# Kernel tuning notes

Hardware: AMD Instinct MI355X
Metric: run time of the kernel (lower is better)

## Reference

```python
import jax, jax.numpy as jnp
import numpy as np
from jax import lax


def _normalizer(x):
    # faithful to: x / norm(x, axis=-1, keepdims=True) + 1e-10
    return x / jnp.linalg.norm(x, axis=-1, keepdims=True) + 1e-10


def setup_inputs() -> dict:
    key = jax.random.key(0)
    k1, k2, k3, k4 = jax.random.split(key, 4)
    Q, D, N, C = 4096, 768, 100000, 1000
    return {
        "feature": jax.random.normal(k1, (Q, D), dtype=jnp.float32),
        "logit": jax.random.normal(k2, (Q, C), dtype=jnp.float32),
        "bank_feas": jax.random.normal(k3, (N, D), dtype=jnp.float32),
        "bank_logits": jax.random.normal(k4, (N, C), dtype=jnp.float32),
        "K": 100,
    }


def reference(feature, logit, bank_feas, bank_logits, K):
    # --- setup(): build bank_guide ---
    bank_confs = jax.nn.logsumexp(bank_logits, axis=-1)          # [N]
    bank_guide = _normalizer(bank_feas) * bank_confs[:, None]    # [N, D]

    # --- forward() ---
    feas_norm = _normalizer(feature)                             # [Q, D]
    energy = jax.nn.logsumexp(logit, axis=-1)                    # [Q]

    # exact kNN inner-product search (faiss IndexFlatIP) = GEMM + top-k
    sims = jnp.einsum("qd,nd->qn", feas_norm, bank_guide)        # [Q, N]
    topk_vals, _ = lax.top_k(sims, K)                            # [Q, K]
    conf = jnp.mean(topk_vals, axis=-1)                          # [Q]

    score = conf * energy
    return -score
```

## Files before the change

### kernel.cpp

```cpp
#include <hip/hip_runtime.h>
#include <hip/hip_bf16.h>

#define QROWS 4096
#define DDIM  768
#define NBANK 100000
#define CDIM  1000
#define KTOP  100
#define NPAD  102400
#define SEGW2 12800
#define LCAP2 4096

typedef float floatx4 __attribute__((ext_vector_type(4)));
typedef short bf16x8 __attribute__((ext_vector_type(8)));

__device__ inline ushort f2bf(float f) {
  uint b = __float_as_uint(f);
  uint r = b + 0x7fffu + ((b >> 16) & 1u);
  return (ushort)(r >> 16);
}
__device__ inline float o16f(ushort u) {
  ushort b = (u & 0x8000) ? (ushort)(u & 0x7fff) : (ushort)~u;
  return __uint_as_float((uint)b << 16);
}

__global__ __launch_bounds__(256) void bank_prep(const float* __restrict__ logits,
                                                 const float* __restrict__ feas,
                                                 ushort* __restrict__ b16) {
  int row = blockIdx.x * 4 + (threadIdx.x >> 6);
  int lane = threadIdx.x & 63;
  if (row >= NPAD) return;
  ushort4* dst = (ushort4*)(b16 + (size_t)row * DDIM);
  if (row >= NBANK) {
#pragma unroll
    for (int j = 0; j < 3; j++) dst[lane + j * 64] = make_ushort4(0, 0, 0, 0);
    return;
  }
  const float4* lp = (const float4*)(logits + (size_t)row * CDIM);
  float4 v[4];
  float m = -3.0e38f;
#pragma unroll
  for (int j = 0; j < 4; j++) {
    int idx = lane + j * 64;
    if (idx < CDIM / 4) {
      v[j] = lp[idx];
      m = fmaxf(m, fmaxf(fmaxf(v[j].x, v[j].y), fmaxf(v[j].z, v[j].w)));
    } else {
      v[j] = make_float4(-3.0e38f, -3.0e38f, -3.0e38f, -3.0e38f);
    }
  }
#pragma unroll
  for (int off = 32; off; off >>= 1) m = fmaxf(m, __shfl_xor(m, off));
  float s = 0.f;
#pragma unroll
  for (int j = 0; j < 4; j++)
    s += __expf(v[j].x - m) + __expf(v[j].y - m) +
         __expf(v[j].z - m) + __expf(v[j].w - m);
#pragma unroll
  for (int off = 32; off; off >>= 1) s += __shfl_xor(s, off);
  float conf = m + __logf(s);
  const float4* fp = (const float4*)(feas + (size_t)row * DDIM);
  float4 w[3];
  float ss = 0.f;
#pragma unroll
  for (int j = 0; j < 3; j++) {
    w[j] = fp[lane + j * 64];
    ss += w[j].x * w[j].x + w[j].y * w[j].y + w[j].z * w[j].z + w[j].w * w[j].w;
  }
#pragma unroll
  for (int off = 32; off; off >>= 1) ss += __shfl_xor(ss, off);
  float scale = conf / sqrtf(ss);
#pragma unroll
  for (int j = 0; j < 3; j++)
    dst[lane + j * 64] = make_ushort4(f2bf(w[j].x * scale), f2bf(w[j].y * scale),
                                      f2bf(w[j].z * scale), f2bf(w[j].w * scale));
}

__global__ __launch_bounds__(256) void lse_rows(const float* __restrict__ x,
                                                float* __restrict__ out,
                                                int nrows, int ncols) {
  int row = blockIdx.x * 4 + (threadIdx.x >> 6);
  int lane = threadIdx.x & 63;
  if (row >= nrows) return;
  const float4* rp = (const float4*)(x + (size_t)row * ncols);
  int n4 = ncols >> 2;
  float4 v[4];
  float m = -3.0e38f;
#pragma unroll
  for (int j = 0; j < 4; j++) {
    int idx = lane + j * 64;
    if (idx < n4) {
      v[j] = rp[idx];
      m = fmaxf(m, fmaxf(fmaxf(v[j].x, v[j].y), fmaxf(v[j].z, v[j].w)));
    } else {
      v[j] = make_float4(-3.0e38f, -3.0e38f, -3.0e38f, -3.0e38f);
    }
  }
#pragma unroll
  for (int off = 32; off; off >>= 1) m = fmaxf(m, __shfl_xor(m, off));
  float s = 0.f;
#pragma unroll
  for (int j = 0; j < 4; j++)
    s += __expf(v[j].x - m) + __expf(v[j].y - m) +
         __expf(v[j].z - m) + __expf(v[j].w - m);
#pragma unroll
  for (int off = 32; off; off >>= 1) s += __shfl_xor(s, off);
  if (lane == 0) out[row] = m + __logf(s);
}

__global__ __launch_bounds__(256) void feat_norm(const float* __restrict__ x,
                                                 ushort* __restrict__ y) {
  int row = blockIdx.x * 4 + (threadIdx.x >> 6);
  int lane = threadIdx.x & 63;
  if (row >= QROWS) return;
  const float4* rp = (const float4*)(x + (size_t)row * DDIM);
  float4 v[3];
  float ss = 0.f;
#pragma unroll
  for (int j = 0; j < 3; j++) {
    v[j] = rp[lane + j * 64];
    ss += v[j].x * v[j].x + v[j].y * v[j].y + v[j].z * v[j].z + v[j].w * v[j].w;
  }
#pragma unroll
  for (int off = 32; off; off >>= 1) ss += __shfl_xor(ss, off);
  float rn = 1.0f / sqrtf(ss);
  ushort4* dst = (ushort4*)(y + (size_t)row * DDIM);
#pragma unroll
  for (int j = 0; j < 3; j++)
    dst[lane + j * 64] = make_ushort4(f2bf(v[j].x * rn), f2bf(v[j].y * rn),
                                      f2bf(v[j].z * rn), f2bf(v[j].w * rn));
}

#define GBM 256
#define GBN 256
#define GBK 64
#define NT  (DDIM / GBK)
#define GNWG ((QROWS / GBM) * (NPAD / GBN))

__device__ inline void load_lds16(const void* g, void* l) {
  __builtin_amdgcn_global_load_lds(
      (const __attribute__((address_space(1))) void*)g,
      (__attribute__((address_space(3))) void*)l, 16, 0, 0);
}

__global__ __launch_bounds__(512, 2) void gemm_sims(const ushort* __restrict__ A,
                                                    const ushort* __restrict__ B,
                                                    ushort* __restrict__ C) {
  __shared__ ushort lds[2 * 32768];
  const int tid = threadIdx.x;
  const int lane = tid & 63;
  const int wid = tid >> 6;
  const int wm = wid >> 2, wn = wid & 3;
  const int lr = lane & 15, lg = lane >> 4;

  int flat = blockIdx.x;
  int wgid = (flat & 7) * (GNWG / 8) + (flat >> 3);
  int sup = wgid >> 4, wi = wgid & 15;
  int q_idx = (sup & 3) * 4 + (wi & 3);
  int n_idx = (sup >> 2) * 4 + (wi >> 2);
  const int qBase = q_idx * GBM;
  const int nBase = n_idx * GBN;

  const int rin = lane >> 3;
  const int cswu = ((lane & 7) ^ rin) << 3;

  auto stageA = [&](int t, int buf) {
#pragma unroll
    for (int r = 0; r < 4; r++) {
      int G = r * 8 + wid;
      int row = qBase + G * 8 + rin;
      load_lds16(A + (size_t)row * DDIM + t * GBK + cswu,
                 lds + buf * 32768 + G * 512 + lane * 8);
    }
  };
  auto stageB = [&](int t, int buf) {
#pragma unroll
    for (int r = 0; r < 4; r++) {
      int G = r * 8 + wid;
      int row = nBase + G * 8 + rin;
      load_lds16(B + (size_t)row * DDIM + t * GBK + cswu,
                 lds + buf * 32768 + 16384 + G * 512 + lane * 8);
    }
  };

  floatx4 acc[8][4] = {};
  const int rsw = (lr & 7) << 3;

  stageA(0, 0); stageB(0, 0); stageA(1, 1); stageB(1, 1);

  for (int s = 0; s < NT; s++) {
    const int buf = s & 1;
    if (s == 0)           asm volatile("s_waitcnt vmcnt(8)" ::: "memory");
    else if (s == NT - 1) asm volatile("s_waitcnt vmcnt(0)" ::: "memory");
    else                  asm volatile("s_waitcnt vmcnt(4)" ::: "memory");
    __builtin_amdgcn_s_barrier();
    __builtin_amdgcn_sched_barrier(0);
    if (s >= 1 && s + 1 < NT) stageA(s + 1, buf ^ 1);
    const ushort* Ab = lds + buf * 32768;
    const ushort* Bb = Ab + 16384;

    bf16x8 bfr[4][2], af[2][2];
#pragma unroll
    for (int n = 0; n < 4; n++)
#pragma unroll
      for (int kk = 0; kk < 2; kk++)
        bfr[n][kk] = *(const bf16x8*)(Bb + (wn * 64 + n * 16 + lr) * 64 +
                                      ((kk * 32 + lg * 8) ^ rsw));
#pragma unroll
    for (int m = 0; m < 2; m++)
#pragma unroll
      for (int kk = 0; kk < 2; kk++)
        af[m][kk] = *(const bf16x8*)(Ab + (wm * 128 + m * 16 + lr) * 64 +
                                     ((kk * 32 + lg * 8) ^ rsw));
    __builtin_amdgcn_s_setprio(1);
#pragma unroll
    for (int m = 0; m < 2; m++)
#pragma unroll
      for (int n = 0; n < 4; n++)
#pragma unroll
        for (int kk = 0; kk < 2; kk++)
          acc[m][n] = __builtin_amdgcn_mfma_f32_16x16x32_bf16(af[m][kk], bfr[n][kk],
                                                              acc[m][n], 0, 0, 0);
    __builtin_amdgcn_s_setprio(0);
    __builtin_amdgcn_s_barrier();
    __builtin_amdgcn_sched_barrier(0);
    if (s + 2 < NT) stageB(s + 2, buf);

#pragma unroll
    for (int q = 1; q < 4; q++) {
      bf16x8 aq[2][2];
#pragma unroll
      for (int m = 0; m < 2; m++)
#pragma unroll
        for (int kk = 0; kk < 2; kk++)
          aq[m][kk] = *(const bf16x8*)(Ab + (wm * 128 + (2 * q + m) * 16 + lr) * 64 +
                                       ((kk * 32 + lg * 8) ^ rsw));
      __builtin_amdgcn_s_setprio(1);
#pragma unroll
      for (int m = 0; m < 2; m++)
#pragma unroll
        for (int n = 0; n < 4; n++)
#pragma unroll
          for (int kk = 0; kk < 2; kk++)
            acc[2 * q + m][n] = __builtin_amdgcn_mfma_f32_16x16x32_bf16(
                aq[m][kk], bfr[n][kk], acc[2 * q + m][n], 0, 0, 0);
      __builtin_amdgcn_s_setprio(0);
    }
  }

#pragma unroll
  for (int m = 0; m < 8; m++)
#pragma unroll
    for (int n = 0; n < 4; n++) {
      int q = qBase + wm * 128 + m * 16 + lg * 4;
      int col = nBase + wn * 64 + n * 16 + lr;
      ushort* cp = C + (size_t)q * NPAD + col;
#pragma unroll
      for (int r = 0; r < 4; r++) cp[(size_t)r * NPAD] = f2bf(acc[m][n][r]);
    }
}

__global__ __launch_bounds__(256) void topk_seg(const ushort* __restrict__ sims,
                                                ushort* __restrict__ cand) {
  __shared__ ushort smax[256];
  __shared__ ushort list[LCAP2];
  __shared__ int shC, shM, ipart[4];
  const int t = threadIdx.x;
  const int lane = t & 63;
  const int q = blockIdx.x >> 3, seg = blockIdx.x & 7;
  const ushort* base = sims + (size_t)q * NPAD + seg * SEGW2;

  uint v[25];
#pragma unroll
  for (int i = 0; i < 6; i++) {
    uint4 w = ((const uint4*)base)[i * 256 + t];
    uint ww[4] = {w.x, w.y, w.z, w.w};
#pragma unroll
    for (int e = 0; e < 4; e++) {
      uint u = ww[e];
      uint mm = ((u >> 15) & 0x00010001u) * 0xffffu;
      v[4 * i + e] = (u ^ mm) | (0x80008000u & ~mm);
    }
    if (seg == 7 && (i * 256 + t) >= 1300) {
      v[4 * i] = 0; v[4 * i + 1] = 0; v[4 * i + 2] = 0; v[4 * i + 3] = 0;
    }
  }
  {
    if (seg == 7) {
      v[24] = 0;
    } else {
      uint u = ((const uint*)base)[6144 + t];
      uint mm = ((u >> 15) & 0x00010001u) * 0xffffu;
      v[24] = (u ^ mm) | (0x80008000u & ~mm);
    }
  }
  uint mx = 0;
#pragma unroll
  for (int i = 0; i < 25; i++) {
    uint a = v[i] & 0xffffu, b = v[i] >> 16;
    mx = a > mx ? a : mx;
    mx = b > mx ? b : mx;
  }
  smax[t] = (ushort)mx;
  if (t == 0) shC = 0;
  __syncthreads();

  uint m0 = smax[lane], m1 = smax[lane + 64], m2 = smax[lane + 128], m3 = smax[lane + 192];
  uint lo = 0, hi = 65536;
  while (hi - lo > 1) {
    uint mid = (lo + hi) >> 1;
    int c = (m0 >= mid) + (m1 >= mid) + (m2 >= mid) + (m3 >= mid);
#pragma unroll
    for (int off = 32; off; off >>= 1) c += __shfl_xor(c, off);
    if (c >= KTOP) lo = mid; else hi = mid;
  }
  const uint L = lo;

  const unsigned long long ltm = (1ull << lane) - 1ull;
  int tot = 0;
#pragma unroll
  for (int i = 0; i < 25; i++) {
    tot += __popcll(__ballot((v[i] & 0xffffu) >= L));
    tot += __popcll(__ballot((v[i] >> 16) >= L));
  }
  int wb = 0;
  if (lane == 0) wb = atomicAdd(&shC, tot);
  wb = __shfl(wb, 0);
  int run = wb;
#pragma unroll
  for (int i = 0; i < 25; i++) {
    uint a = v[i] & 0xffffu, b = v[i] >> 16;
    unsigned long long ma = __ballot(a >= L);
    if (a >= L) { int p = run + __popcll(ma & ltm); if (p < LCAP2) list[p] = (ushort)a; }
    run += __popcll(ma);
    unsigned long long mb = __ballot(b >= L);
    if (b >= L) { int p = run + __popcll(mb & ltm); if (p < LCAP2) list[p] = (ushort)b; }
    run += __popcll(mb);
  }
  __syncthreads();
  const int C = shC;

  uint Tkey;
  if (C <= LCAP2) {
    uint lo2 = L, hi2 = 65536;
    while (hi2 - lo2 > 1) {
      uint mid = (lo2 + hi2) >> 1;
      int c = 0;
      for (int i = lane; i < C; i += 64) c += ((uint)list[i] >= mid) ? 1 : 0;
#pragma unroll
      for (int off = 32; off; off >>= 1) c += __shfl_xor(c, off);
      if (c >= KTOP) lo2 = mid; else hi2 = mid;
    }
    Tkey = lo2;
  } else {
    uint lo2 = L, hi2 = 65536;
    while (hi2 - lo2 > 1) {
      uint mid = (lo2 + hi2) >> 1;
      int c = 0;
#pragma unroll
      for (int i = 0; i < 25; i++) {
        c += ((v[i] & 0xffffu) >= mid) ? 1 : 0;
        c += ((v[i] >> 16) >= mid) ? 1 : 0;
      }
#pragma unroll
      for (int off = 32; off; off >>= 1) c += __shfl_xor(c, off);
      __syncthreads();
      if (lane == 0) ipart[t >> 6] = c;
      __syncthreads();
      c = ipart[0] + ipart[1] + ipart[2] + ipart[3];
      if (c >= KTOP) lo2 = mid; else hi2 = mid;
    }
    Tkey = lo2;
  }

  if (t == 0) shM = 0;
  __syncthreads();
  ushort* dst = cand + (size_t)q * 1024 + seg * 128;
  if (C <= LCAP2) {
    for (int i = t; i < C; i += 256) {
      uint u = list[i];
      if (u > Tkey) { int p = atomicAdd(&shM, 1); dst[p] = (ushort)u; }
    }
  } else {
#pragma unroll
    for (int i = 0; i < 25; i++) {
      uint a = v[i] & 0xffffu, b = v[i] >> 16;
      if (a > Tkey) { int p = atomicAdd(&shM, 1); dst[p] = (ushort)a; }
      if (b > Tkey) { int p = atomicAdd(&shM, 1); dst[p] = (ushort)b; }
    }
  }
  __syncthreads();
  for (int i = shM + t; i < KTOP; i += 256) dst[i] = (ushort)Tkey;
}

__global__ __launch_bounds__(64) void topk_fin(const ushort* __restrict__ cand,
                                               const float* __restrict__ energy,
                                               float* __restrict__ out) {
  const int q = blockIdx.x;
  const int t = threadIdx.x;
  const ushort* row = cand + (size_t)q * 1024;
  ushort kk[16];
#pragma unroll
  for (int s = 0; s < 8; s++) {
    kk[2 * s]     = row[s * 128 + t];
    kk[2 * s + 1] = (t + 64 < KTOP) ? row[s * 128 + 64 + t] : (ushort)0;
  }
  uint lo = 0, hi = 65536;
  while (hi - lo > 1) {
    uint mid = (lo + hi) >> 1;
    int c = 0;
#pragma unroll
    for (int i = 0; i < 16; i++) c += ((uint)kk[i] >= mid) ? 1 : 0;
#pragma unroll
    for (int off = 32; off; off >>= 1) c += __shfl_xor(c, off);
    if (c >= KTOP) lo = mid; else hi = mid;
  }
  const uint T = lo;
  float s = 0.f;
  int m = 0;
#pragma unroll
  for (int i = 0; i < 16; i++) {
    if ((uint)kk[i] > T) { s += o16f(kk[i]); m++; }
  }
#pragma unroll
  for (int off = 32; off; off >>= 1) {
    s += __shfl_xor(s, off);
    m += __shfl_xor(m, off);
  }
  if (t == 0) {
    float total = s + (float)(KTOP - m) * o16f((ushort)T);
    out[q] = -(total * (1.0f / KTOP)) * energy[q];
  }
}

extern "C" void kernel_launch(void* const* d_in, const int* in_sizes, int n_in,
                              void* d_out, int out_size, void* d_ws, size_t ws_size,
                              hipStream_t stream) {
  const float* feature     = (const float*)d_in[0];
  const float* logit       = (const float*)d_in[1];
  const float* bank_feas   = (const float*)d_in[2];
  const float* bank_logits = (const float*)d_in[3];
  float* out = (float*)d_out;

  char* ws = (char*)d_ws;
  size_t off = 0;
  auto take = [&](size_t bytes) -> char* {
    char* p = ws + off;
    off = (off + bytes + 255) & ~(size_t)255;
    return p;
  };
  float*  energy = (float*)take((size_t)QROWS * 4);
  ushort* a16    = (ushort*)take((size_t)QROWS * DDIM * 2);
  ushort* b16    = (ushort*)take((size_t)NPAD * DDIM * 2);
  ushort* sims   = (ushort*)take((size_t)QROWS * NPAD * 2);
  ushort* cand   = (ushort*)take((size_t)QROWS * 1024 * 2);
  if (off > ws_size) return;

  bank_prep<<<dim3(NPAD / 4), dim3(256), 0, stream>>>(bank_logits, bank_feas, b16);
  lse_rows <<<dim3(QROWS / 4), dim3(256), 0, stream>>>(logit, energy, QROWS, CDIM);
  feat_norm<<<dim3(QROWS / 4), dim3(256), 0, stream>>>(feature, a16);
  gemm_sims<<<dim3(GNWG), dim3(512), 0, stream>>>(a16, b16, sims);
  topk_seg <<<dim3(QROWS * 8), dim3(256), 0, stream>>>(sims, cand);
  topk_fin <<<dim3(QROWS), dim3(64), 0, stream>>>(cand, energy, out);
}
```

Before: 1.347 ms.

## Restructure GEMM main loop into fine-grained phased load/compute pipeline

Rewrites the GEMM main loop so each K-step is split into four phases. Each phase issues half of the next A or B tile's LDS loads, then runs one quarter of the MFMA work, with barriers and waitcnts placed per phase. Launch bounds drop the two-blocks-per-CU hint. The fused bank preparation kernel is split into a logsumexp pass and a separate scale/convert pass, and the top-k threshold searches now count with ballot/popcount instead of shuffle reductions. The extra barriers and the occupancy change could offset the finer overlap, and the split bank prep adds a launch plus an extra conf buffer round trip.

```diff
diff --git a/kernel.cpp b/kernel.cpp
--- a/kernel.cpp
+++ b/kernel.cpp
@@ -21,58 +21,6 @@
 __device__ inline float o16f(ushort u) {
   ushort b = (u & 0x8000) ? (ushort)(u & 0x7fff) : (ushort)~u;
   return __uint_as_float((uint)b << 16);
-}
-
-__global__ __launch_bounds__(256) void bank_prep(const float* __restrict__ logits,
-                                                 const float* __restrict__ feas,
-                                                 ushort* __restrict__ b16) {
-  int row = blockIdx.x * 4 + (threadIdx.x >> 6);
-  int lane = threadIdx.x & 63;
-  if (row >= NPAD) return;
-  ushort4* dst = (ushort4*)(b16 + (size_t)row * DDIM);
-  if (row >= NBANK) {
-#pragma unroll
-    for (int j = 0; j < 3; j++) dst[lane + j * 64] = make_ushort4(0, 0, 0, 0);
-    return;
-  }
-  const float4* lp = (const float4*)(logits + (size_t)row * CDIM);
-  float4 v[4];
-  float m = -3.0e38f;
-#pragma unroll
-  for (int j = 0; j < 4; j++) {
-    int idx = lane + j * 64;
-    if (idx < CDIM / 4) {
-      v[j] = lp[idx];
-      m = fmaxf(m, fmaxf(fmaxf(v[j].x, v[j].y), fmaxf(v[j].z, v[j].w)));
-    } else {
-      v[j] = make_float4(-3.0e38f, -3.0e38f, -3.0e38f, -3.0e38f);
-    }
-  }
-#pragma unroll
-  for (int off = 32; off; off >>= 1) m = fmaxf(m, __shfl_xor(m, off));
-  float s = 0.f;
-#pragma unroll
-  for (int j = 0; j < 4; j++)
-    s += __expf(v[j].x - m) + __expf(v[j].y - m) +
-         __expf(v[j].z - m) + __expf(v[j].w - m);
-#pragma unroll
-  for (int off = 32; off; off >>= 1) s += __shfl_xor(s, off);
-  float conf = m + __logf(s);
-  const float4* fp = (const float4*)(feas + (size_t)row * DDIM);
-  float4 w[3];
-  float ss = 0.f;
-#pragma unroll
-  for (int j = 0; j < 3; j++) {
-    w[j] = fp[lane + j * 64];
-    ss += w[j].x * w[j].x + w[j].y * w[j].y + w[j].z * w[j].z + w[j].w * w[j].w;
-  }
-#pragma unroll
-  for (int off = 32; off; off >>= 1) ss += __shfl_xor(ss, off);
-  float scale = conf / sqrtf(ss);
-#pragma unroll
-  for (int j = 0; j < 3; j++)
-    dst[lane + j * 64] = make_ushort4(f2bf(w[j].x * scale), f2bf(w[j].y * scale),
-                                      f2bf(w[j].z * scale), f2bf(w[j].w * scale));
 }
 
 __global__ __launch_bounds__(256) void lse_rows(const float* __restrict__ x,
@@ -107,6 +55,35 @@
   if (lane == 0) out[row] = m + __logf(s);
 }
 
+__global__ __launch_bounds__(256) void bank_sc(const float* __restrict__ feas,
+                                               const float* __restrict__ conf,
+                                               ushort* __restrict__ b16) {
+  int row = blockIdx.x * 4 + (threadIdx.x >> 6);
+  int lane = threadIdx.x & 63;
+  if (row >= NPAD) return;
+  ushort4* dst = (ushort4*)(b16 + (size_t)row * DDIM);
+  if (row >= NBANK) {
+#pragma unroll
+    for (int j = 0; j < 3; j++) dst[lane + j * 64] = make_ushort4(0, 0, 0, 0);
+    return;
+  }
+  const float4* fp = (const float4*)(feas + (size_t)row * DDIM);
+  float4 w[3];
+  float ss = 0.f;
+#pragma unroll
+  for (int j = 0; j < 3; j++) {
+    w[j] = fp[lane + j * 64];
+    ss += w[j].x * w[j].x + w[j].y * w[j].y + w[j].z * w[j].z + w[j].w * w[j].w;
+  }
+#pragma unroll
+  for (int off = 32; off; off >>= 1) ss += __shfl_xor(ss, off);
+  float s = conf[row] / sqrtf(ss);
+#pragma unroll
+  for (int j = 0; j < 3; j++)
+    dst[lane + j * 64] = make_ushort4(f2bf(w[j].x * s), f2bf(w[j].y * s),
+                                      f2bf(w[j].z * s), f2bf(w[j].w * s));
+}
+
 __global__ __launch_bounds__(256) void feat_norm(const float* __restrict__ x,
                                                  ushort* __restrict__ y) {
   int row = blockIdx.x * 4 + (threadIdx.x >> 6);
@@ -142,9 +119,39 @@
       (__attribute__((address_space(3))) void*)l, 16, 0, 0);
 }
 
-__global__ __launch_bounds__(512, 2) void gemm_sims(const ushort* __restrict__ A,
-                                                    const ushort* __restrict__ B,
-                                                    ushort* __restrict__ C) {
+#define PHASE(BUF, Q, LOADB, STAGE_STMT, VM_STMT)                              \
+  {                                                                            \
+    const ushort* Ab = lds + (BUF) * 32768;                                    \
+    if (LOADB) {                                                               \
+      const ushort* Bb = Ab + 16384;                                           \
+      _Pragma("unroll") for (int n = 0; n < 4; n++)                            \
+        _Pragma("unroll") for (int kk = 0; kk < 2; kk++)                       \
+          bfr[n][kk] = *(const bf16x8*)(Bb + (wn * 64 + n * 16 + lr) * 64 +    \
+                                        ((kk * 32 + lg * 8) ^ rsw));           \
+    }                                                                          \
+    bf16x8 af[2][2];                                                           \
+    _Pragma("unroll") for (int m = 0; m < 2; m++)                              \
+      _Pragma("unroll") for (int kk = 0; kk < 2; kk++)                         \
+        af[m][kk] = *(const bf16x8*)(Ab + (wm * 128 + (2 * (Q) + m) * 16 + lr) \
+                                     * 64 + ((kk * 32 + lg * 8) ^ rsw));       \
+    STAGE_STMT;                                                                \
+    __builtin_amdgcn_s_barrier();                                              \
+    asm volatile("s_waitcnt lgkmcnt(0)" ::: "memory");                         \
+    __builtin_amdgcn_sched_barrier(0);                                         \
+    __builtin_amdgcn_s_setprio(1);                                             \
+    _Pragma("unroll") for (int m = 0; m < 2; m++)                              \
+      _Pragma("unroll") for (int n = 0; n < 4; n++)                            \
+        _Pragma("unroll") for (int kk = 0; kk < 2; kk++)                       \
+          acc[2 * (Q) + m][n] = __builtin_amdgcn_mfma_f32_16x16x32_bf16(       \
+              af[m][kk], bfr[n][kk], acc[2 * (Q) + m][n], 0, 0, 0);            \
+    __builtin_amdgcn_s_setprio(0);                                             \
+    VM_STMT;                                                                   \
+    __builtin_amdgcn_s_barrier();                                              \
+  }
+
+__global__ __launch_bounds__(512) void gemm_sims(const ushort* __restrict__ A,
+                                                 const ushort* __restrict__ B,
+                                                 ushort* __restrict__ C) {
   __shared__ ushort lds[2 * 32768];
   const int tid = threadIdx.x;
   const int lane = tid & 63;
@@ -162,89 +169,55 @@
 
   const int rin = lane >> 3;
   const int cswu = ((lane & 7) ^ rin) << 3;
-
-  auto stageA = [&](int t, int buf) {
-#pragma unroll
-    for (int r = 0; r < 4; r++) {
-      int G = r * 8 + wid;
-      int row = qBase + G * 8 + rin;
-      load_lds16(A + (size_t)row * DDIM + t * GBK + cswu,
-                 lds + buf * 32768 + G * 512 + lane * 8);
+  const int rsw = (lr & 7) << 3;
+
+  auto stageAh = [&](int t, int h) {
+    if (t < NT) {
+#pragma unroll
+      for (int r = 2 * h; r < 2 * h + 2; r++) {
+        int G = r * 8 + wid;
+        int row = qBase + G * 8 + rin;
+        load_lds16(A + (size_t)row * DDIM + t * GBK + cswu,
+                   lds + (t & 1) * 32768 + G * 512 + lane * 8);
+      }
     }
   };
-  auto stageB = [&](int t, int buf) {
-#pragma unroll
-    for (int r = 0; r < 4; r++) {
-      int G = r * 8 + wid;
-      int row = nBase + G * 8 + rin;
-      load_lds16(B + (size_t)row * DDIM + t * GBK + cswu,
-                 lds + buf * 32768 + 16384 + G * 512 + lane * 8);
+  auto stageBh = [&](int t, int h) {
+    if (t < NT) {
+#pragma unroll
+      for (int r = 2 * h; r < 2 * h + 2; r++) {
+        int G = r * 8 + wid;
+        int row = nBase + G * 8 + rin;
+        load_lds16(B + (size_t)row * DDIM + t * GBK + cswu,
+                   lds + (t & 1) * 32768 + 16384 + G * 512 + lane * 8);
+      }
     }
   };
 
   floatx4 acc[8][4] = {};
-  const int rsw = (lr & 7) << 3;
-
-  stageA(0, 0); stageB(0, 0); stageA(1, 1); stageB(1, 1);
-
-  for (int s = 0; s < NT; s++) {
-    const int buf = s & 1;
-    if (s == 0)           asm volatile("s_waitcnt vmcnt(8)" ::: "memory");
-    else if (s == NT - 1) asm volatile("s_waitcnt vmcnt(0)" ::: "memory");
-    else                  asm volatile("s_waitcnt vmcnt(4)" ::: "memory");
-    __builtin_amdgcn_s_barrier();
-    __builtin_amdgcn_sched_barrier(0);
-    if (s >= 1 && s + 1 < NT) stageA(s + 1, buf ^ 1);
-    const ushort* Ab = lds + buf * 32768;
-    const ushort* Bb = Ab + 16384;
-
-    bf16x8 bfr[4][2], af[2][2];
-#pragma unroll
-    for (int n = 0; n < 4; n++)
-#pragma unroll
-      for (int kk = 0; kk < 2; kk++)
-        bfr[n][kk] = *(const bf16x8*)(Bb + (wn * 64 + n * 16 + lr) * 64 +
-                                      ((kk * 32 + lg * 8) ^ rsw));
-#pragma unroll
-    for (int m = 0; m < 2; m++)
-#pragma unroll
-      for (int kk = 0; kk < 2; kk++)
-        af[m][kk] = *(const bf16x8*)(Ab + (wm * 128 + m * 16 + lr) * 64 +
-                                     ((kk * 32 + lg * 8) ^ rsw));
-    __builtin_amdgcn_s_setprio(1);
-#pragma unroll
-    for (int m = 0; m < 2; m++)
-#pragma unroll
-      for (int n = 0; n < 4; n++)
-#pragma unroll
-        for (int kk = 0; kk < 2; kk++)
-          acc[m][n] = __builtin_amdgcn_mfma_f32_16x16x32_bf16(af[m][kk], bfr[n][kk],
-                                                              acc[m][n], 0, 0, 0);
-    __builtin_amdgcn_s_setprio(0);
-    __builtin_amdgcn_s_barrier();
-    __builtin_amdgcn_sched_barrier(0);
-    if (s + 2 < NT) stageB(s + 2, buf);
-
-#pragma unroll
-    for (int q = 1; q < 4; q++) {
-      bf16x8 aq[2][2];
-#pragma unroll
-      for (int m = 0; m < 2; m++)
-#pragma unroll
-        for (int kk = 0; kk < 2; kk++)
-          aq[m][kk] = *(const bf16x8*)(Ab + (wm * 128 + (2 * q + m) * 16 + lr) * 64 +
-                                       ((kk * 32 + lg * 8) ^ rsw));
-      __builtin_amdgcn_s_setprio(1);
-#pragma unroll
-      for (int m = 0; m < 2; m++)
-#pragma unroll
-        for (int n = 0; n < 4; n++)
-#pragma unroll
-          for (int kk = 0; kk < 2; kk++)
-            acc[2 * q + m][n] = __builtin_amdgcn_mfma_f32_16x16x32_bf16(
-                aq[m][kk], bfr[n][kk], acc[2 * q + m][n], 0, 0, 0);
-      __builtin_amdgcn_s_setprio(0);
-    }
+  bf16x8 bfr[4][2];
+
+  stageBh(0, 0); stageBh(0, 1);
+  stageAh(0, 0); stageAh(0, 1);
+  stageBh(1, 0); stageBh(1, 1);
+  asm volatile("s_waitcnt vmcnt(4)" ::: "memory");
+  __builtin_amdgcn_s_barrier();
+
+#pragma unroll 1
+  for (int i = 0; i < NT / 2; i++) {
+    const int t0 = 2 * i;
+    const bool last = (i == NT / 2 - 1);
+    PHASE(0, 0, true,  stageAh(t0 + 1, 0), );
+    PHASE(0, 1, false, stageAh(t0 + 1, 1), );
+    PHASE(0, 2, false, stageBh(t0 + 2, 0), );
+    PHASE(0, 3, false, stageBh(t0 + 2, 1),
+          if (last) { asm volatile("s_waitcnt vmcnt(0)" ::: "memory"); }
+          else      { asm volatile("s_waitcnt vmcnt(4)" ::: "memory"); });
+    PHASE(1, 0, true,  stageAh(t0 + 2, 0), );
+    PHASE(1, 1, false, stageAh(t0 + 2, 1), );
+    PHASE(1, 2, false, stageBh(t0 + 3, 0), );
+    PHASE(1, 3, false, stageBh(t0 + 3, 1),
+          if (!last) { asm volatile("s_waitcnt vmcnt(4)" ::: "memory"); });
   }
 
 #pragma unroll
@@ -308,9 +281,8 @@
   uint lo = 0, hi = 65536;
   while (hi - lo > 1) {
     uint mid = (lo + hi) >> 1;
-    int c = (m0 >= mid) + (m1 >= mid) + (m2 >= mid) + (m3 >= mid);
-#pragma unroll
-    for (int off = 32; off; off >>= 1) c += __shfl_xor(c, off);
+    int c = __popcll(__ballot(m0 >= mid)) + __popcll(__ballot(m1 >= mid)) +
+            __popcll(__ballot(m2 >= mid)) + __popcll(__ballot(m3 >= mid));
     if (c >= KTOP) lo = mid; else hi = mid;
   }
   const uint L = lo;
@@ -345,9 +317,10 @@
     while (hi2 - lo2 > 1) {
       uint mid = (lo2 + hi2) >> 1;
       int c = 0;
-      for (int i = lane; i < C; i += 64) c += ((uint)list[i] >= mid) ? 1 : 0;
-#pragma unroll
-      for (int off = 32; off; off >>= 1) c += __shfl_xor(c, off);
+      for (int j = 0; j < C; j += 64) {
+        bool p = (j + lane < C) && ((uint)list[j + lane] >= mid);
+        c += __popcll(__ballot(p));
+      }
       if (c >= KTOP) lo2 = mid; else hi2 = mid;
     }
     Tkey = lo2;
@@ -449,13 +422,15 @@
     return p;
   };
   float*  energy = (float*)take((size_t)QROWS * 4);
+  float*  conf   = (float*)take((size_t)NPAD * 4);
   ushort* a16    = (ushort*)take((size_t)QROWS * DDIM * 2);
   ushort* b16    = (ushort*)take((size_t)NPAD * DDIM * 2);
   ushort* sims   = (ushort*)take((size_t)QROWS * NPAD * 2);
   ushort* cand   = (ushort*)take((size_t)QROWS * 1024 * 2);
   if (off > ws_size) return;
 
-  bank_prep<<<dim3(NPAD / 4), dim3(256), 0, stream>>>(bank_logits, bank_feas, b16);
+  lse_rows <<<dim3((NBANK + 3) / 4), dim3(256), 0, stream>>>(bank_logits, conf, NBANK, CDIM);
+  bank_sc  <<<dim3(NPAD / 4), dim3(256), 0, stream>>>(bank_feas, conf, b16);
   lse_rows <<<dim3(QROWS / 4), dim3(256), 0, stream>>>(logit, energy, QROWS, CDIM);
   feat_norm<<<dim3(QROWS / 4), dim3(256), 0, stream>>>(feature, a16);
   gemm_sims<<<dim3(GNWG), dim3(512), 0, stream>>>(a16, b16, sims);
```

New measurement: 1.122 ms, median of 3. 1.2x faster.
